# Optimization experiments

Hardware: AMD Instinct MI355X
Metric: run time of the kernel (lower is better)

Reference implementation:

```python
import jax, jax.numpy as jnp
import numpy as np

B, S, H = 1, 2048, 1024
NH, KVH, HD = 16, 4, 64
E, TOPK, F = 8, 2, 2048
EPS = 1e-5
THETA = 10000.0


def setup_inputs() -> dict:
    key = jax.random.key(0)
    ks = jax.random.split(key, 12)
    s = 0.02
    return {
        "hidden_states": jax.random.normal(ks[0], (B, S, H), jnp.float32),
        "position_ids": jnp.arange(S, dtype=jnp.int64).reshape(1, S),
        "ln1_w": jnp.ones((H,), jnp.float32),
        "ln2_w": jnp.ones((H,), jnp.float32),
        "wq": jax.random.normal(ks[1], (NH * HD, H), jnp.float32) * s,
        "wk": jax.random.normal(ks[2], (KVH * HD, H), jnp.float32) * s,
        "wv": jax.random.normal(ks[3], (KVH * HD, H), jnp.float32) * s,
        "wo": jax.random.normal(ks[4], (H, NH * HD), jnp.float32) * s,
        "gate_w": jax.random.normal(ks[5], (E, H), jnp.float32) * s,
        "w1": jax.random.normal(ks[6], (E, F, H), jnp.float32) * s,
        "w2": jax.random.normal(ks[7], (E, H, F), jnp.float32) * s,
        "w3": jax.random.normal(ks[8], (E, F, H), jnp.float32) * s,
    }


def rmsnorm(x, w, eps=EPS):
    xf = x.astype(jnp.float32)
    v = jnp.mean(xf * xf, axis=-1, keepdims=True)
    return (xf * jax.lax.rsqrt(v + eps)).astype(x.dtype) * w


def rotate_half(x):
    x1, x2 = jnp.split(x, 2, axis=-1)
    return jnp.concatenate([-x2, x1], axis=-1)


def attention(x, position_ids, wq, wk, wv, wo):
    q = (x @ wq.T).reshape(B, S, NH, HD).transpose(0, 2, 1, 3)   # [B,NH,S,HD]
    k = (x @ wk.T).reshape(B, S, KVH, HD).transpose(0, 2, 1, 3)  # [B,KVH,S,HD]
    v = (x @ wv.T).reshape(B, S, KVH, HD).transpose(0, 2, 1, 3)
    inv_freq = 1.0 / (THETA ** (jnp.arange(0, HD, 2, dtype=jnp.float32) / HD))
    ang = position_ids.astype(jnp.float32)[:, :, None] * inv_freq  # [B,S,HD/2]
    emb = jnp.concatenate([ang, ang], axis=-1)                     # [B,S,HD]
    cos = jnp.cos(emb)[:, None]                                    # [B,1,S,HD]
    sin = jnp.sin(emb)[:, None]
    q = q * cos + rotate_half(q) * sin
    k = k * cos + rotate_half(k) * sin
    rep = NH // KVH
    k = jnp.repeat(k, rep, axis=1)
    v = jnp.repeat(v, rep, axis=1)
    scores = jnp.einsum("bhqd,bhkd->bhqk", q, k) / np.sqrt(HD).astype(np.float32)
    causal = jnp.tril(jnp.ones((S, S), bool))
    scores = jnp.where(causal, scores, jnp.finfo(scores.dtype).min)
    attn = jax.nn.softmax(scores, axis=-1)
    ctx = jnp.einsum("bhqk,bhkd->bhqd", attn, v)
    ctx = ctx.transpose(0, 2, 1, 3).reshape(B, S, NH * HD)
    return ctx @ wo.T


def moe(x, gate_w, w1, w2, w3):
    xt = x.reshape(-1, H)                                  # [T,H]
    router_logits = xt @ gate_w.T                          # [T,E]
    probs = jax.nn.softmax(router_logits.astype(jnp.float32), axis=-1)
    topw, topi = jax.lax.top_k(probs, TOPK)                # [T,K]
    topw = topw / jnp.sum(topw, axis=-1, keepdims=True)
    topw = topw.astype(x.dtype)
    # combine weights per expert: [T,E]
    cw = jnp.sum(topw[..., None] * jax.nn.one_hot(topi, E, dtype=x.dtype), axis=1)
    h1 = jnp.einsum("th,efh->etf", xt, w1)
    h3 = jnp.einsum("th,efh->etf", xt, w3)
    g = jax.nn.silu(h1) * h3                               # [E,T,F]
    y = jnp.einsum("etf,ehf->eth", g, w2)                  # [E,T,H]
    out = jnp.einsum("eth,te->th", y, cw)
    return out.reshape(B, S, H), router_logits


def reference(hidden_states, position_ids, ln1_w, ln2_w, wq, wk, wv, wo,
              gate_w, w1, w2, w3):
    residual = hidden_states
    h = rmsnorm(hidden_states, ln1_w)
    h = attention(h, position_ids, wq, wk, wv, wo)
    h = residual + h
    residual = h
    h = rmsnorm(h, ln2_w)
    h, router_logits = moe(h, gate_w, w1, w2, w3)
    h = residual + h
    return h, router_logits
```

## Files before the change

### kernel.cpp

```cpp
#include <hip/hip_runtime.h>
#include <hip/hip_bf16.h>
#include <cstdint>

typedef unsigned short u16;
typedef __attribute__((ext_vector_type(8))) short bh8;
typedef __attribute__((ext_vector_type(4))) short sh4;
typedef __attribute__((ext_vector_type(4))) float fx4;

#define NTOK 2048
#define HDIM 1024
#define NE 8
#define FDIM 2048

#define VMCNT(n) asm volatile("s_waitcnt vmcnt(" #n ")" ::: "memory")
#define LGKM0()  asm volatile("s_waitcnt lgkmcnt(0)" ::: "memory")
#define SBAR()   __builtin_amdgcn_s_barrier()
#define SCB()    __builtin_amdgcn_sched_barrier(0)

__device__ __forceinline__ u16 f2bf(float f) {
    __hip_bfloat16 h = __float2bfloat16(f);
    return __builtin_bit_cast(u16, h);
}

__device__ __forceinline__ void gll16(const void* g, void* l) {
    __builtin_amdgcn_global_load_lds(
        (const __attribute__((address_space(1))) void*)g,
        (__attribute__((address_space(3))) void*)l, 16, 0, 0);
}

#define N8_WQ 131072
#define N8_WK 32768
#define N8_WV 32768
#define N8_WO 131072
#define N8_W  2097152
#define B0q 0
#define B1k (B0q + N8_WQ)
#define B2v (B1k + N8_WK)
#define B3o (B2v + N8_WV)
#define B4a (B3o + N8_WO)
#define B5b (B4a + N8_W)
#define B6c (B5b + N8_W)
#define N8TOT (B6c + N8_W)
#define N8QKVO B4a
#define N8_W13 (2 * N8_W)

__device__ __forceinline__ void conv8_nt(const float* __restrict__ src, size_t li,
                                         u16* __restrict__ dst, size_t di) {
    const fx4 a = __builtin_nontemporal_load((const fx4*)&src[li]);
    const fx4 b = __builtin_nontemporal_load((const fx4*)&src[li + 4]);
    bh8 o;
    #pragma unroll
    for (int j = 0; j < 4; ++j) {
        o[j]     = (short)f2bf(a[j]);
        o[j + 4] = (short)f2bf(b[j]);
    }
    __builtin_nontemporal_store(o, (bh8*)&dst[di]);
}

__device__ __forceinline__ void conv8(const float* __restrict__ src, size_t li,
                                      u16* __restrict__ dst, size_t di) {
    const fx4 a = *(const fx4*)&src[li];
    const fx4 b = *(const fx4*)&src[li + 4];
    bh8 o;
    #pragma unroll
    for (int j = 0; j < 4; ++j) {
        o[j]     = (short)f2bf(a[j]);
        o[j + 4] = (short)f2bf(b[j]);
    }
    *(bh8*)&dst[di] = o;
}

__global__ __launch_bounds__(256)
void prologue_k(const float* __restrict__ wq, const float* __restrict__ wk,
                const float* __restrict__ wv, const float* __restrict__ wo,
                u16* __restrict__ arena,
                float* __restrict__ cosT, float* __restrict__ sinT,
                const float* __restrict__ X, const float* __restrict__ W,
                u16* __restrict__ O) {
    const int bid = blockIdx.x;
    const int tid = threadIdx.x;
    if (bid < 256) {
        int i = bid * 256 + tid;
        const int stride = 256 * 256;
        for (; i < N8QKVO; i += stride) {
            const float* src;
            int base;
            if (i < B1k)      { src = wq; base = B0q; }
            else if (i < B2v) { src = wk; base = B1k; }
            else if (i < B3o) { src = wv; base = B2v; }
            else              { src = wo; base = B3o; }
            conv8(src, (size_t)(i - base) * 8, arena, (size_t)i * 8);
        }
        return;
    }
    if (bid < 512) {
        const int idx = (bid - 256) * 256 + tid;
        const int t = idx >> 5, i = idx & 31;
        const float freq = powf(10000.0f, -(float)i * (1.0f / 32.0f));
        const float ang = (float)t * freq;
        float s, c;
        sincosf(ang, &s, &c);
        cosT[idx] = c;
        sinT[idx] = s;
        return;
    }
    const int t = bid - 512;
    const fx4 v = *(const fx4*)&X[(size_t)t * HDIM + tid * 4];
    float ss = v[0]*v[0] + v[1]*v[1] + v[2]*v[2] + v[3]*v[3];
    #pragma unroll
    for (int o = 1; o < 64; o <<= 1) ss += __shfl_xor(ss, o);
    __shared__ float red[4];
    if ((tid & 63) == 0) red[tid >> 6] = ss;
    __syncthreads();
    const float inv = rsqrtf((red[0] + red[1] + red[2] + red[3]) * (1.0f / HDIM) + 1e-5f);
    const fx4 w = *(const fx4*)&W[tid * 4];
    sh4 o4;
    #pragma unroll
    for (int i = 0; i < 4; ++i) o4[i] = (short)f2bf(v[i] * inv * w[i]);
    *(sh4*)&O[(size_t)t * HDIM + tid * 4] = o4;
}

__global__ __launch_bounds__(256)
void rmsnorm2_router_k(const float* __restrict__ X, const float* __restrict__ W,
                       const float* __restrict__ GW, u16* __restrict__ O,
                       float* __restrict__ LOGI) {
    const int t = blockIdx.x;
    const int tid = threadIdx.x;
    const fx4 v = *(const fx4*)&X[(size_t)t * HDIM + tid * 4];
    float ss = v[0]*v[0] + v[1]*v[1] + v[2]*v[2] + v[3]*v[3];
    #pragma unroll
    for (int o = 1; o < 64; o <<= 1) ss += __shfl_xor(ss, o);
    __shared__ float red[4];
    if ((tid & 63) == 0) red[tid >> 6] = ss;
    __syncthreads();
    const float inv = rsqrtf((red[0] + red[1] + red[2] + red[3]) * (1.0f / HDIM) + 1e-5f);
    const fx4 w = *(const fx4*)&W[tid * 4];
    fx4 xn;
    #pragma unroll
    for (int i = 0; i < 4; ++i) xn[i] = v[i] * inv * w[i];
    sh4 o4;
    #pragma unroll
    for (int i = 0; i < 4; ++i) o4[i] = (short)f2bf(xn[i]);
    *(sh4*)&O[(size_t)t * HDIM + tid * 4] = o4;

    float part[NE];
    #pragma unroll
    for (int e = 0; e < NE; ++e) {
        const fx4 g = *(const fx4*)&GW[(size_t)e * HDIM + tid * 4];
        part[e] = g[0]*xn[0] + g[1]*xn[1] + g[2]*xn[2] + g[3]*xn[3];
    }
    #pragma unroll
    for (int e = 0; e < NE; ++e)
        #pragma unroll
        for (int o = 1; o < 64; o <<= 1) part[e] += __shfl_xor(part[e], o);
    __shared__ float red8[4][NE];
    if ((tid & 63) == 0) {
        #pragma unroll
        for (int e = 0; e < NE; ++e) red8[tid >> 6][e] = part[e];
    }
    __syncthreads();
    if (tid < NE)
        LOGI[(size_t)t * NE + tid] = red8[0][tid] + red8[1][tid] + red8[2][tid] + red8[3][tid];
}

__global__ __launch_bounds__(256)
void router_topk_k(const float* __restrict__ LOGI, int* __restrict__ counts,
                   int* __restrict__ tokslot, float* __restrict__ wtb) {
    const int t = blockIdx.x * 256 + threadIdx.x;
    float l[NE];
    #pragma unroll
    for (int e = 0; e < NE; ++e) l[e] = LOGI[(size_t)t * NE + e];
    int i0 = 0;
    #pragma unroll
    for (int e = 1; e < NE; ++e) if (l[e] > l[i0]) i0 = e;
    int i1 = (i0 == 0) ? 1 : 0;
    #pragma unroll
    for (int e = 0; e < NE; ++e) if (e != i0 && l[e] > l[i1]) i1 = e;
    float e1 = __expf(l[i1] - l[i0]);
    float w0 = 1.0f / (1.0f + e1);
    float w1 = 1.0f - w0;
    int p0 = atomicAdd(&counts[i0], 1);
    tokslot[i0 * NTOK + p0] = t * 2;
    wtb[i0 * NTOK + p0] = w0;
    int p1 = atomicAdd(&counts[i1], 1);
    tokslot[i1 * NTOK + p1] = t * 2 + 1;
    wtb[i1 * NTOK + p1] = w1;
}

__global__ __launch_bounds__(256)
void qkv_gemm_k(const u16* __restrict__ A, const u16* __restrict__ Bw,
                u16* __restrict__ Qb, u16* __restrict__ Kb, u16* __restrict__ VTb,
                const float* __restrict__ cosT, const float* __restrict__ sinT) {
    __shared__ u16 As[4][64 * 32];
    __shared__ u16 Bs[4][64 * 32];

    const int tid = threadIdx.x;
    const int lane = tid & 63;
    const int wid = tid >> 6;
    const int lrow = lane & 15, lgrp = lane >> 4;
    const int wm = wid * 16;
    const int soff = (lgrp ^ ((lrow >> 1) & 3)) * 8;

    const int m0 = blockIdx.y * 64;
    const int nt = blockIdx.x;
    const int n0 = nt * 64;

    const int gseg = ((tid & 3) ^ ((tid >> 3) & 3)) * 8;
    const u16* apg = A + (size_t)(m0 + (tid >> 2)) * 1024 + gseg;
    const u16* bpg = Bw + (size_t)(n0 + (tid >> 2)) * 1024 + gseg;

    fx4 acc[4];
    #pragma unroll
    for (int i = 0; i < 4; ++i) acc[i] = fx4{0.f, 0.f, 0.f, 0.f};

#define G_STG(BUF, KK) gll16(apg + (KK), &As[BUF][wid * 512]); \
                       gll16(bpg + (KK), &Bs[BUF][wid * 512]);
#define G_CMP(BUF)                                                             \
    {                                                                          \
        const bh8 af = *(const bh8*)&As[BUF][(wm + lrow) * 32 + soff];         \
        _Pragma("unroll")                                                      \
        for (int ni = 0; ni < 4; ++ni) {                                       \
            const bh8 bf = *(const bh8*)&Bs[BUF][(ni * 16 + lrow) * 32 + soff];\
            acc[ni] = __builtin_amdgcn_mfma_f32_16x16x32_bf16(af, bf, acc[ni], 0, 0, 0); \
        }                                                                      \
    }
#define G_PHASE(BUF_ST, KOFF, BUF_CM)                                          \
    { const int kn = (k0 + (KOFF) < 1024) ? k0 + (KOFF) : 0; G_STG(BUF_ST, kn) } \
    VMCNT(6); SBAR(); SCB();                                                   \
    G_CMP(BUF_CM)                                                              \
    LGKM0(); SBAR();

    G_STG(0, 0) G_STG(1, 32) G_STG(2, 64)
    for (int k0 = 0; k0 < 1024; k0 += 128) {
        G_PHASE(3, 96, 0)
        G_PHASE(0, 128, 1)
        G_PHASE(1, 160, 2)
        G_PHASE(2, 192, 3)
    }
    VMCNT(0);
#undef G_STG
#undef G_CMP
#undef G_PHASE

    if (nt < 20) {
        u16* dst = (nt < 16) ? Qb : Kb;
        const int N = (nt < 16) ? 1024 : 256;
        const int cb = (nt < 16) ? n0 : (nt - 16) * 64;
        #pragma unroll
        for (int j = 0; j < 4; ++j) {
            const int r = m0 + wm + lgrp * 4 + j;
            #pragma unroll
            for (int ni = 0; ni < 2; ++ni) {
                const int d = ni * 16 + lrow;
                const float cv = cosT[r * 32 + d];
                const float sv = sinT[r * 32 + d];
                const float v0 = acc[ni][j];
                const float v1 = acc[ni + 2][j];
                dst[(size_t)r * N + cb + d]      = f2bf(v0 * cv - v1 * sv);
                dst[(size_t)r * N + cb + d + 32] = f2bf(v1 * cv + v0 * sv);
            }
        }
    } else {
        #pragma unroll
        for (int ni = 0; ni < 4; ++ni) {
            const int c = (nt - 20) * 64 + ni * 16 + lrow;
            const int r = m0 + wm + lgrp * 4;
            sh4 o4;
            #pragma unroll
            for (int j = 0; j < 4; ++j) o4[j] = (short)f2bf(acc[ni][j]);
            *(sh4*)&VTb[(size_t)c * NTOK + r] = o4;
        }
    }
}

template<int EPI>
__global__ __launch_bounds__(256)
void gemm_bt(const u16* __restrict__ A, const u16* __restrict__ B,
             u16* __restrict__ Cb, float* __restrict__ Cf,
             const int N, const int K,
             const float* __restrict__ aux0, const float* __restrict__ aux1) {
    __shared__ u16 As[4][64 * 32];
    __shared__ u16 Bs[4][64 * 32];

    const int tid = threadIdx.x;
    const int lane = tid & 63;
    const int wid = tid >> 6;
    const int lrow = lane & 15, lgrp = lane >> 4;
    const int wm = wid * 16;
    const int soff = (lgrp ^ ((lrow >> 1) & 3)) * 8;

    const int m0 = blockIdx.y * 64;
    const int n0 = blockIdx.x * 64;

    const int gseg = ((tid & 3) ^ ((tid >> 3) & 3)) * 8;
    const u16* apg = A + (size_t)(m0 + (tid >> 2)) * K + gseg;
    const u16* bpg = B + (size_t)(n0 + (tid >> 2)) * K + gseg;

    fx4 acc[4];
    #pragma unroll
    for (int i = 0; i < 4; ++i) acc[i] = fx4{0.f, 0.f, 0.f, 0.f};

#define G_STG(BUF, KK) gll16(apg + (KK), &As[BUF][wid * 512]); \
                       gll16(bpg + (KK), &Bs[BUF][wid * 512]);
#define G_CMP(BUF)                                                             \
    {                                                                          \
        const bh8 af = *(const bh8*)&As[BUF][(wm + lrow) * 32 + soff];         \
        _Pragma("unroll")                                                      \
        for (int ni = 0; ni < 4; ++ni) {                                       \
            const bh8 bf = *(const bh8*)&Bs[BUF][(ni * 16 + lrow) * 32 + soff];\
            acc[ni] = __builtin_amdgcn_mfma_f32_16x16x32_bf16(af, bf, acc[ni], 0, 0, 0); \
        }                                                                      \
    }
#define G_PHASE(BUF_ST, KOFF, BUF_CM)                                          \
    { const int kn = (k0 + (KOFF) < K) ? k0 + (KOFF) : 0; G_STG(BUF_ST, kn) }  \
    VMCNT(6); SBAR(); SCB();                                                   \
    G_CMP(BUF_CM)                                                              \
    LGKM0(); SBAR();

    G_STG(0, 0) G_STG(1, 32) G_STG(2, 64)
    for (int k0 = 0; k0 < K; k0 += 128) {
        G_PHASE(3, 96, 0)
        G_PHASE(0, 128, 1)
        G_PHASE(1, 160, 2)
        G_PHASE(2, 192, 3)
    }
    VMCNT(0);
#undef G_STG
#undef G_CMP
#undef G_PHASE

    #pragma unroll
    for (int j = 0; j < 4; ++j) {
        const int r = m0 + wm + lgrp * 4 + j;
        #pragma unroll
        for (int ni = 0; ni < 4; ++ni) {
            const int c = n0 + ni * 16 + lrow;
            const float v = acc[ni][j];
            if (EPI == 1) Cf[(size_t)r * N + c] = v + aux0[(size_t)r * N + c];
        }
    }
}

__global__ __launch_bounds__(256)
void attn_conv_k(const u16* __restrict__ Q, const u16* __restrict__ Kg,
                 const u16* __restrict__ VTg, float* __restrict__ pacc,
                 float* __restrict__ pl,
                 const float* __restrict__ w1, const float* __restrict__ w3,
                 u16* __restrict__ arena_moe) {
    if (blockIdx.z >= 4) {
        const int bid = (blockIdx.z - 4) * 512 + blockIdx.y * 32 + blockIdx.x;
        const int stride = 1024 * 256;
        int i = bid * 256 + threadIdx.x;
        #pragma unroll 1
        for (int k = 0; k < 4; ++k) {
            #pragma unroll
            for (int u = 0; u < 4; ++u) {
                const int ii = i + u * stride;
                const float* s = (ii < N8_W) ? w1 : w3;
                const size_t li = (size_t)(ii < N8_W ? ii : ii - N8_W) * 8;
                const size_t di = (size_t)(ii < N8_W ? ii : ii + N8_W) * 8;
                conv8_nt(s, li, arena_moe, di);
            }
            i += 4 * stride;
        }
        return;
    }

    const int qt = blockIdx.x;
    const int h = blockIdx.y;
    const int c = blockIdx.z;
    if (c * 8 > qt) return;
    const int t0 = c * 8;
    const int tend = min(qt + 1, t0 + 8);
    const int kvh = h >> 2;

    const int tid = threadIdx.x;
    const int lane = tid & 63;
    const int wid = tid >> 6;
    const int lrow = lane & 15, lgrp = lane >> 4;

    __shared__ u16 Ks[64 * 66];
    __shared__ u16 Vs[64 * 66];
    __shared__ u16 Ps[4][16 * 66];

    const int qbase = qt * 64 + wid * 16;

    bh8 qf[2];
    #pragma unroll
    for (int kf = 0; kf < 2; ++kf)
        qf[kf] = *(const bh8*)&Q[(size_t)(qbase + lrow) * 1024 + h * 64 + kf * 32 + lgrp * 8];

    fx4 acc[4];
    #pragma unroll
    for (int ni = 0; ni < 4; ++ni) acc[ni] = fx4{0.f, 0.f, 0.f, 0.f};
    float lsum[4];
    #pragma unroll
    for (int j = 0; j < 4; ++j) lsum[j] = 0.f;

    const int srow = tid >> 2;
    const int sseg = (tid & 3) * 16;

    size_t gk = (size_t)(t0 * 64 + srow) * 256 + kvh * 64 + sseg;
    size_t gv = (size_t)(kvh * 64 + srow) * NTOK + t0 * 64 + sseg;
    bh8 kva = *(const bh8*)&Kg[gk];
    bh8 kvb = *(const bh8*)&Kg[gk + 8];
    bh8 vva = *(const bh8*)&VTg[gv];
    bh8 vvb = *(const bh8*)&VTg[gv + 8];

    for (int it = t0; it < tend; ++it) {
        const int kv0 = it * 64;
        __syncthreads();
        *(bh8*)&Ks[srow * 66 + sseg]     = kva;
        *(bh8*)&Ks[srow * 66 + sseg + 8] = kvb;
        *(bh8*)&Vs[srow * 66 + sseg]     = vva;
        *(bh8*)&Vs[srow * 66 + sseg + 8] = vvb;
        __syncthreads();

        const int itn = (it + 1 < tend) ? it + 1 : it;
        const size_t gk2 = (size_t)(itn * 64 + srow) * 256 + kvh * 64 + sseg;
        const size_t gv2 = (size_t)(kvh * 64 + srow) * NTOK + itn * 64 + sseg;
        kva = *(const bh8*)&Kg[gk2];
        kvb = *(const bh8*)&Kg[gk2 + 8];
        vva = *(const bh8*)&VTg[gv2];
        vvb = *(const bh8*)&VTg[gv2 + 8];

        fx4 s[4];
        #pragma unroll
        for (int nf = 0; nf < 4; ++nf) s[nf] = fx4{0.f, 0.f, 0.f, 0.f};
        #pragma unroll
        for (int kf = 0; kf < 2; ++kf) {
            #pragma unroll
            for (int nf = 0; nf < 4; ++nf) {
                const bh8 kfr = *(const bh8*)&Ks[(nf * 16 + lrow) * 66 + kf * 32 + lgrp * 8];
                s[nf] = __builtin_amdgcn_mfma_f32_16x16x32_bf16(qf[kf], kfr, s[nf], 0, 0, 0);
            }
        }

        #pragma unroll
        for (int nf = 0; nf < 4; ++nf)
            #pragma unroll
            for (int j = 0; j < 4; ++j) {
                const int qr = qbase + lgrp * 4 + j;
                const int kp = kv0 + nf * 16 + lrow;
                float p = __expf(fmaf(s[nf][j], 0.125f, -24.0f));
                p = (kp > qr) ? 0.f : p;
                s[nf][j] = p;
                lsum[j] += p;
            }

        u16* pw = Ps[wid];
        #pragma unroll
        for (int nf = 0; nf < 4; ++nf)
            #pragma unroll
            for (int j = 0; j < 4; ++j)
                pw[(lgrp * 4 + j) * 66 + nf * 16 + lrow] = f2bf(s[nf][j]);

        #pragma unroll
        for (int kf = 0; kf < 2; ++kf) {
            const bh8 pa = *(const bh8*)&pw[lrow * 66 + kf * 32 + lgrp * 8];
            #pragma unroll
            for (int ni = 0; ni < 4; ++ni) {
                const bh8 vb = *(const bh8*)&Vs[(ni * 16 + lrow) * 66 + kf * 32 + lgrp * 8];
                acc[ni] = __builtin_amdgcn_mfma_f32_16x16x32_bf16(pa, vb, acc[ni], 0, 0, 0);
            }
        }
    }

    #pragma unroll
    for (int j = 0; j < 4; ++j) {
        float l = lsum[j];
        #pragma unroll
        for (int o = 1; o < 16; o <<= 1) l += __shfl_xor(l, o);
        lsum[j] = l;
    }

    #pragma unroll
    for (int j = 0; j < 4; ++j) {
        const int r = qbase + lgrp * 4 + j;
        const size_t base = ((size_t)(h * NTOK + r) * 4 + c) * 64;
        #pragma unroll
        for (int ni = 0; ni < 4; ++ni)
            pacc[base + ni * 16 + lrow] = acc[ni][j];
        if (lrow == 0)
            pl[(size_t)(h * NTOK + r) * 4 + c] = lsum[j];
    }
}

__global__ __launch_bounds__(256)
void attn_combine_k(const float* __restrict__ pacc, const float* __restrict__ pl,
                    u16* __restrict__ O) {
    const int idx = blockIdx.x * 4 + (threadIdx.x >> 6);
    const int d = threadIdx.x & 63;
    const int h = idx >> 11;
    const int qrow = idx & 2047;
    const int nch = (qrow >> 9) + 1;

    float den = 0.f, num = 0.f;
    for (int c = 0; c < nch; ++c) {
        den += pl[(size_t)idx * 4 + c];
        num += pacc[((size_t)idx * 4 + c) * 64 + d];
    }
    O[(size_t)qrow * 1024 + h * 64 + d] = f2bf(num / den);
}

__global__ __launch_bounds__(256)
void moe_up_k(const u16* __restrict__ X, const u16* __restrict__ W1b,
              const u16* __restrict__ W3b, const int* __restrict__ counts,
              const int* __restrict__ tokslot, u16* __restrict__ G,
              const float* __restrict__ w2, u16* __restrict__ w2b) {
    if (blockIdx.z == 8) {
        const int bid = blockIdx.y * 16 + blockIdx.x;
        const int stride = 512 * 256;
        int i = bid * 256 + threadIdx.x;
        #pragma unroll 1
        for (int k = 0; k < 4; ++k) {
            #pragma unroll
            for (int u = 0; u < 4; ++u)
                conv8_nt(w2, (size_t)(i + u * stride) * 8, w2b, (size_t)(i + u * stride) * 8);
            i += 4 * stride;
        }
        return;
    }

    const int e = blockIdx.z;
    const int cnt = counts[e];
    const int m0 = blockIdx.y * 64;
    if (m0 >= cnt) return;
    const int n0 = blockIdx.x * 128;

    __shared__ u16 As[4][64 * 32];
    __shared__ u16 B1s[4][128 * 32];
    __shared__ u16 B3s[4][128 * 32];

    const int tid = threadIdx.x;
    const int lane = tid & 63, wid = tid >> 6;
    const int wm = (wid >> 1) * 32, wn = (wid & 1) * 64;
    const int lrow = lane & 15, lgrp = lane >> 4;
    const int soff = (lgrp ^ ((lrow >> 1) & 3)) * 8;

    const int gseg = ((tid & 3) ^ ((tid >> 3) & 3)) * 8;
    const int arow = m0 + (tid >> 2);
    const int tok = (arow < cnt) ? (tokslot[e * NTOK + arow] >> 1) : 0;
    const u16* apg = X + (size_t)tok * HDIM + gseg;
    const size_t eoff = (size_t)e * FDIM * HDIM;
    const u16* b1pg = W1b + eoff + (size_t)(n0 + (tid >> 2)) * HDIM + gseg;
    const u16* b3pg = W3b + eoff + (size_t)(n0 + (tid >> 2)) * HDIM + gseg;
    const size_t rr = (size_t)64 * HDIM;

    fx4 acc1[2][4], acc3[2][4];
    #pragma unroll
    for (int i = 0; i < 2; ++i)
        #pragma unroll
        for (int j = 0; j < 4; ++j) {
            acc1[i][j] = fx4{0.f, 0.f, 0.f, 0.f};
            acc3[i][j] = fx4{0.f, 0.f, 0.f, 0.f};
        }

#define U_STG(BUF, KK)                                          \
    gll16(apg + (KK), &As[BUF][wid * 512]);                     \
    gll16(b1pg + (KK), &B1s[BUF][wid * 512]);                   \
    gll16(b1pg + rr + (KK), &B1s[BUF][2048 + wid * 512]);       \
    gll16(b3pg + (KK), &B3s[BUF][wid * 512]);                   \
    gll16(b3pg + rr + (KK), &B3s[BUF][2048 + wid * 512]);

#define U_CMP(BUF)                                                                   \
    {                                                                                \
        bh8 af[2], b1f[4], b3f[4];                                                   \
        _Pragma("unroll")                                                            \
        for (int mi = 0; mi < 2; ++mi)                                               \
            af[mi] = *(const bh8*)&As[BUF][(wm + mi * 16 + lrow) * 32 + soff];       \
        _Pragma("unroll")                                                            \
        for (int ni = 0; ni < 4; ++ni) {                                             \
            b1f[ni] = *(const bh8*)&B1s[BUF][(wn + ni * 16 + lrow) * 32 + soff];     \
            b3f[ni] = *(const bh8*)&B3s[BUF][(wn + ni * 16 + lrow) * 32 + soff];     \
        }                                                                            \
        _Pragma("unroll")                                                            \
        for (int mi = 0; mi < 2; ++mi)                                               \
            _Pragma("unroll")                                                        \
            for (int ni = 0; ni < 4; ++ni) {                                         \
                acc1[mi][ni] = __builtin_amdgcn_mfma_f32_16x16x32_bf16(af[mi], b1f[ni], acc1[mi][ni], 0, 0, 0); \
                acc3[mi][ni] = __builtin_amdgcn_mfma_f32_16x16x32_bf16(af[mi], b3f[ni], acc3[mi][ni], 0, 0, 0); \
            }                                                                        \
    }

#define U_PHASE(BUF_ST, KOFF, BUF_CM)                                          \
    { const int kn = (k0 + (KOFF) < HDIM) ? k0 + (KOFF) : 0; U_STG(BUF_ST, kn) } \
    VMCNT(15); SBAR(); SCB();                                                  \
    U_CMP(BUF_CM)                                                              \
    LGKM0(); SBAR();

    U_STG(0, 0) U_STG(1, 32) U_STG(2, 64)
    for (int k0 = 0; k0 < HDIM; k0 += 128) {
        U_PHASE(3, 96, 0)
        U_PHASE(0, 128, 1)
        U_PHASE(1, 160, 2)
        U_PHASE(2, 192, 3)
    }
    VMCNT(0);
#undef U_STG
#undef U_CMP
#undef U_PHASE

    #pragma unroll
    for (int mi = 0; mi < 2; ++mi)
        #pragma unroll
        for (int j = 0; j < 4; ++j) {
            const int r = m0 + wm + mi * 16 + lgrp * 4 + j;
            if (r < cnt) {
                #pragma unroll
                for (int ni = 0; ni < 4; ++ni) {
                    const int c = n0 + wn + ni * 16 + lrow;
                    const float h1 = acc1[mi][ni][j];
                    const float h3 = acc3[mi][ni][j];
                    const float gv = h1 / (1.0f + __expf(-h1)) * h3;
                    G[((size_t)e * NTOK + r) * FDIM + c] = f2bf(gv);
                }
            }
        }
}

__global__ __launch_bounds__(256)
void moe_down_k(const u16* __restrict__ G, const u16* __restrict__ W2b,
                const int* __restrict__ counts, const int* __restrict__ tokslot,
                const float* __restrict__ wtb, float* __restrict__ MO) {
    const int e = blockIdx.z;
    const int cnt = counts[e];
    const int m0 = blockIdx.y * 64;
    if (m0 >= cnt) return;
    const int n0 = blockIdx.x * 64;

    __shared__ u16 As[4][64 * 32];
    __shared__ u16 Bs[4][64 * 32];

    const int tid = threadIdx.x;
    const int lane = tid & 63;
    const int wid = tid >> 6;
    const int lrow = lane & 15, lgrp = lane >> 4;
    const int wm = wid * 16;
    const int soff = (lgrp ^ ((lrow >> 1) & 3)) * 8;

    const int gseg = ((tid & 3) ^ ((tid >> 3) & 3)) * 8;
    const u16* apg = G + ((size_t)e * NTOK + m0 + (tid >> 2)) * FDIM + gseg;
    const u16* bpg = W2b + (size_t)e * HDIM * FDIM + (size_t)(n0 + (tid >> 2)) * FDIM + gseg;

    fx4 acc[4];
    #pragma unroll
    for (int i = 0; i < 4; ++i) acc[i] = fx4{0.f, 0.f, 0.f, 0.f};

#define D_STG(BUF, KK) gll16(apg + (KK), &As[BUF][wid * 512]); \
                       gll16(bpg + (KK), &Bs[BUF][wid * 512]);
#define D_CMP(BUF)                                                             \
    {                                                                          \
        const bh8 af = *(const bh8*)&As[BUF][(wm + lrow) * 32 + soff];         \
        _Pragma("unroll")                                                      \
        for (int ni = 0; ni < 4; ++ni) {                                       \
            const bh8 bf = *(const bh8*)&Bs[BUF][(ni * 16 + lrow) * 32 + soff];\
            acc[ni] = __builtin_amdgcn_mfma_f32_16x16x32_bf16(af, bf, acc[ni], 0, 0, 0); \
        }                                                                      \
    }
#define D_PHASE(BUF_ST, KOFF, BUF_CM)                                          \
    { const int kn = (k0 + (KOFF) < FDIM) ? k0 + (KOFF) : 0; D_STG(BUF_ST, kn) } \
    VMCNT(6); SBAR(); SCB();                                                   \
    D_CMP(BUF_CM)                                                              \
    LGKM0(); SBAR();

    D_STG(0, 0) D_STG(1, 32) D_STG(2, 64)
    for (int k0 = 0; k0 < FDIM; k0 += 128) {
        D_PHASE(3, 96, 0)
        D_PHASE(0, 128, 1)
        D_PHASE(1, 160, 2)
        D_PHASE(2, 192, 3)
    }
    VMCNT(0);
#undef D_STG
#undef D_CMP
#undef D_PHASE

    #pragma unroll
    for (int j = 0; j < 4; ++j) {
        const int r = m0 + wm + lgrp * 4 + j;
        if (r < cnt) {
            const int ts = tokslot[e * NTOK + r];
            const float wgt = wtb[e * NTOK + r];
            const int tt = ts >> 1;
            const int sl = ts & 1;
            #pragma unroll
            for (int ni = 0; ni < 4; ++ni) {
                const int c = n0 + ni * 16 + lrow;
                MO[((size_t)sl * NTOK + tt) * HDIM + c] = acc[ni][j] * wgt;
            }
        }
    }
}

__global__ __launch_bounds__(256)
void final_add_k(const float* __restrict__ A, const float* __restrict__ B0,
                 const float* __restrict__ B1, float* __restrict__ O) {
    const size_t i = ((size_t)blockIdx.x * 256 + threadIdx.x) * 4;
    const fx4 a = *(const fx4*)&A[i];
    const fx4 b = *(const fx4*)&B0[i];
    const fx4 c = *(const fx4*)&B1[i];
    fx4 r;
    #pragma unroll
    for (int k = 0; k < 4; ++k) r[k] = a[k] + b[k] + c[k];
    *(fx4*)&O[i] = r;
}

extern "C" void kernel_launch(void* const* d_in, const int* in_sizes, int n_in,
                              void* d_out, int out_size, void* d_ws, size_t ws_size,
                              hipStream_t stream) {
    const float* x   = (const float*)d_in[0];
    const float* ln1 = (const float*)d_in[2];
    const float* ln2 = (const float*)d_in[3];
    const float* wq  = (const float*)d_in[4];
    const float* wk  = (const float*)d_in[5];
    const float* wv  = (const float*)d_in[6];
    const float* wo  = (const float*)d_in[7];
    const float* gw  = (const float*)d_in[8];
    const float* w1  = (const float*)d_in[9];
    const float* w2  = (const float*)d_in[10];
    const float* w3  = (const float*)d_in[11];

    float* out_h = (float*)d_out;
    float* out_logits = out_h + (size_t)NTOK * HDIM;

    uint8_t* wsb = (uint8_t*)d_ws;
    size_t off = 0;
    auto alloc = [&](size_t bytes) -> void* {
        void* ptr = wsb + off;
        off = (off + bytes + 255) & ~(size_t)255;
        return ptr;
    };
    u16*   xn1    = (u16*)alloc((size_t)NTOK * HDIM * 2);
    u16*   qb     = (u16*)alloc((size_t)NTOK * 1024 * 2);
    u16*   kb     = (u16*)alloc((size_t)NTOK * 256 * 2);
    u16*   vbt    = (u16*)alloc((size_t)256 * NTOK * 2);
    u16*   ctxb   = (u16*)alloc((size_t)NTOK * 1024 * 2);
    float* hattn  = (float*)alloc((size_t)NTOK * HDIM * 4);
    u16*   xn2    = (u16*)alloc((size_t)NTOK * HDIM * 2);
    float* cosT   = (float*)alloc((size_t)NTOK * 32 * 4);
    float* sinT   = (float*)alloc((size_t)NTOK * 32 * 4);
    int*   counts = (int*)alloc(NE * 4);
    int*   tokslot= (int*)alloc((size_t)NE * NTOK * 4);
    float* wtb    = (float*)alloc((size_t)NE * NTOK * 4);
    u16*   gbuf   = (u16*)alloc((size_t)NE * NTOK * FDIM * 2);
    float* moeb   = (float*)alloc((size_t)2 * NTOK * HDIM * 4);
    u16*   arena  = (u16*)alloc((size_t)N8TOT * 8 * 2);
    u16*   w1b    = arena + (size_t)B4a * 8;
    u16*   w2b    = arena + (size_t)B5b * 8;
    u16*   w3b    = arena + (size_t)B6c * 8;
    u16*   wob    = arena + (size_t)B3o * 8;

    float* pacc = (float*)gbuf;
    float* pl   = pacc + (size_t)16 * NTOK * 4 * 64;

    hipMemsetAsync(counts, 0, NE * 4, stream);

    prologue_k<<<2560, 256, 0, stream>>>(wq, wk, wv, wo, arena, cosT, sinT, x, ln1, xn1);
    qkv_gemm_k<<<dim3(24, 32), 256, 0, stream>>>(xn1, arena, qb, kb, vbt, cosT, sinT);
    attn_conv_k<<<dim3(32, 16, 6), 256, 0, stream>>>(qb, kb, vbt, pacc, pl,
                                                     w1, w3, arena + (size_t)B4a * 8);
    attn_combine_k<<<8192, 256, 0, stream>>>(pacc, pl, ctxb);
    gemm_bt<1><<<dim3(16, 32), 256, 0, stream>>>(ctxb, wob, nullptr, hattn, 1024, 1024, x, nullptr);
    rmsnorm2_router_k<<<NTOK, 256, 0, stream>>>(hattn, ln2, gw, xn2, out_logits);
    router_topk_k<<<8, 256, 0, stream>>>(out_logits, counts, tokslot, wtb);
    moe_up_k<<<dim3(16, 32, NE + 1), 256, 0, stream>>>(xn2, w1b, w3b, counts, tokslot, gbuf,
                                                       w2, w2b);
    moe_down_k<<<dim3(16, 32, NE), 256, 0, stream>>>(gbuf, w2b, counts, tokslot, wtb, moeb);
    final_add_k<<<NTOK, 256, 0, stream>>>(hattn, moeb, moeb + (size_t)NTOK * HDIM, out_h);
}
```

Before: 338.7 us.

## Use atomic work-stealing for weight conversion inside attention and MoE-up kernels

New measurement: 414.5 us. 22.4% more time.

```diff
diff --git a/kernel.cpp b/kernel.cpp
--- a/kernel.cpp
+++ b/kernel.cpp
@@ -43,6 +43,9 @@
 #define N8TOT (B6c + N8_W)
 #define N8QKVO B4a
 #define N8_W13 (2 * N8_W)
+#define CHUNK_G8 1024
+#define NCHUNK_W13 (N8_W13 / CHUNK_G8)
+#define NCHUNK_W2  (N8_W / CHUNK_G8)
 
 __device__ __forceinline__ void conv8_nt(const float* __restrict__ src, size_t li,
                                          u16* __restrict__ dst, size_t di) {
@@ -346,143 +349,143 @@
                  const u16* __restrict__ VTg, float* __restrict__ pacc,
                  float* __restrict__ pl,
                  const float* __restrict__ w1, const float* __restrict__ w3,
-                 u16* __restrict__ arena_moe) {
-    if (blockIdx.z >= 4) {
-        const int bid = (blockIdx.z - 4) * 512 + blockIdx.y * 32 + blockIdx.x;
-        const int stride = 1024 * 256;
-        int i = bid * 256 + threadIdx.x;
-        #pragma unroll 1
-        for (int k = 0; k < 4; ++k) {
-            #pragma unroll
-            for (int u = 0; u < 4; ++u) {
-                const int ii = i + u * stride;
-                const float* s = (ii < N8_W) ? w1 : w3;
-                const size_t li = (size_t)(ii < N8_W ? ii : ii - N8_W) * 8;
-                const size_t di = (size_t)(ii < N8_W ? ii : ii + N8_W) * 8;
-                conv8_nt(s, li, arena_moe, di);
-            }
-            i += 4 * stride;
-        }
-        return;
-    }
-
+                 u16* __restrict__ arena_moe, int* __restrict__ ctr) {
     const int qt = blockIdx.x;
     const int h = blockIdx.y;
     const int c = blockIdx.z;
-    if (c * 8 > qt) return;
-    const int t0 = c * 8;
-    const int tend = min(qt + 1, t0 + 8);
-    const int kvh = h >> 2;
-
     const int tid = threadIdx.x;
-    const int lane = tid & 63;
-    const int wid = tid >> 6;
-    const int lrow = lane & 15, lgrp = lane >> 4;
-
-    __shared__ u16 Ks[64 * 66];
-    __shared__ u16 Vs[64 * 66];
-    __shared__ u16 Ps[4][16 * 66];
-
-    const int qbase = qt * 64 + wid * 16;
-
-    bh8 qf[2];
-    #pragma unroll
-    for (int kf = 0; kf < 2; ++kf)
-        qf[kf] = *(const bh8*)&Q[(size_t)(qbase + lrow) * 1024 + h * 64 + kf * 32 + lgrp * 8];
-
-    fx4 acc[4];
-    #pragma unroll
-    for (int ni = 0; ni < 4; ++ni) acc[ni] = fx4{0.f, 0.f, 0.f, 0.f};
-    float lsum[4];
-    #pragma unroll
-    for (int j = 0; j < 4; ++j) lsum[j] = 0.f;
-
-    const int srow = tid >> 2;
-    const int sseg = (tid & 3) * 16;
-
-    size_t gk = (size_t)(t0 * 64 + srow) * 256 + kvh * 64 + sseg;
-    size_t gv = (size_t)(kvh * 64 + srow) * NTOK + t0 * 64 + sseg;
-    bh8 kva = *(const bh8*)&Kg[gk];
-    bh8 kvb = *(const bh8*)&Kg[gk + 8];
-    bh8 vva = *(const bh8*)&VTg[gv];
-    bh8 vvb = *(const bh8*)&VTg[gv + 8];
-
-    for (int it = t0; it < tend; ++it) {
-        const int kv0 = it * 64;
+    __shared__ int sh_ch;
+
+    if (c * 8 <= qt) {
+        const int t0 = c * 8;
+        const int tend = min(qt + 1, t0 + 8);
+        const int kvh = h >> 2;
+
+        const int lane = tid & 63;
+        const int wid = tid >> 6;
+        const int lrow = lane & 15, lgrp = lane >> 4;
+
+        __shared__ u16 Ks[64 * 66];
+        __shared__ u16 Vs[64 * 66];
+        __shared__ u16 Ps[4][16 * 66];
+
+        const int qbase = qt * 64 + wid * 16;
+
+        bh8 qf[2];
+        #pragma unroll
+        for (int kf = 0; kf < 2; ++kf)
+            qf[kf] = *(const bh8*)&Q[(size_t)(qbase + lrow) * 1024 + h * 64 + kf * 32 + lgrp * 8];
+
+        fx4 acc[4];
+        #pragma unroll
+        for (int ni = 0; ni < 4; ++ni) acc[ni] = fx4{0.f, 0.f, 0.f, 0.f};
+        float lsum[4];
+        #pragma unroll
+        for (int j = 0; j < 4; ++j) lsum[j] = 0.f;
+
+        const int srow = tid >> 2;
+        const int sseg = (tid & 3) * 16;
+
+        size_t gk = (size_t)(t0 * 64 + srow) * 256 + kvh * 64 + sseg;
+        size_t gv = (size_t)(kvh * 64 + srow) * NTOK + t0 * 64 + sseg;
+        bh8 kva = *(const bh8*)&Kg[gk];
+        bh8 kvb = *(const bh8*)&Kg[gk + 8];
+        bh8 vva = *(const bh8*)&VTg[gv];
+        bh8 vvb = *(const bh8*)&VTg[gv + 8];
+
+        for (int it = t0; it < tend; ++it) {
+            const int kv0 = it * 64;
+            __syncthreads();
+            *(bh8*)&Ks[srow * 66 + sseg]     = kva;
+            *(bh8*)&Ks[srow * 66 + sseg + 8] = kvb;
+            *(bh8*)&Vs[srow * 66 + sseg]     = vva;
+            *(bh8*)&Vs[srow * 66 + sseg + 8] = vvb;
+            __syncthreads();
+
+            const int itn = (it + 1 < tend) ? it + 1 : it;
+            const size_t gk2 = (size_t)(itn * 64 + srow) * 256 + kvh * 64 + sseg;
+            const size_t gv2 = (size_t)(kvh * 64 + srow) * NTOK + itn * 64 + sseg;
+            kva = *(const bh8*)&Kg[gk2];
+            kvb = *(const bh8*)&Kg[gk2 + 8];
+            vva = *(const bh8*)&VTg[gv2];
+            vvb = *(const bh8*)&VTg[gv2 + 8];
+
+            fx4 s[4];
+            #pragma unroll
+            for (int nf = 0; nf < 4; ++nf) s[nf] = fx4{0.f, 0.f, 0.f, 0.f};
+            #pragma unroll
+            for (int kf = 0; kf < 2; ++kf) {
+                #pragma unroll
+                for (int nf = 0; nf < 4; ++nf) {
+                    const bh8 kfr = *(const bh8*)&Ks[(nf * 16 + lrow) * 66 + kf * 32 + lgrp * 8];
+                    s[nf] = __builtin_amdgcn_mfma_f32_16x16x32_bf16(qf[kf], kfr, s[nf], 0, 0, 0);
+                }
+            }
+
+            #pragma unroll
+            for (int nf = 0; nf < 4; ++nf)
+                #pragma unroll
+                for (int j = 0; j < 4; ++j) {
+                    const int qr = qbase + lgrp * 4 + j;
+                    const int kp = kv0 + nf * 16 + lrow;
+                    float p = __expf(fmaf(s[nf][j], 0.125f, -24.0f));
+                    p = (kp > qr) ? 0.f : p;
+                    s[nf][j] = p;
+                    lsum[j] += p;
+                }
+
+            u16* pw = Ps[wid];
+            #pragma unroll
+            for (int nf = 0; nf < 4; ++nf)
+                #pragma unroll
+                for (int j = 0; j < 4; ++j)
+                    pw[(lgrp * 4 + j) * 66 + nf * 16 + lrow] = f2bf(s[nf][j]);
+
+            #pragma unroll
+            for (int kf = 0; kf < 2; ++kf) {
+                const bh8 pa = *(const bh8*)&pw[lrow * 66 + kf * 32 + lgrp * 8];
+                #pragma unroll
+                for (int ni = 0; ni < 4; ++ni) {
+                    const bh8 vb = *(const bh8*)&Vs[(ni * 16 + lrow) * 66 + kf * 32 + lgrp * 8];
+                    acc[ni] = __builtin_amdgcn_mfma_f32_16x16x32_bf16(pa, vb, acc[ni], 0, 0, 0);
+                }
+            }
+        }
+
+        #pragma unroll
+        for (int j = 0; j < 4; ++j) {
+            float l = lsum[j];
+            #pragma unroll
+            for (int o = 1; o < 16; o <<= 1) l += __shfl_xor(l, o);
+            lsum[j] = l;
+        }
+
+        #pragma unroll
+        for (int j = 0; j < 4; ++j) {
+            const int r = qbase + lgrp * 4 + j;
+            const size_t base = ((size_t)(h * NTOK + r) * 4 + c) * 64;
+            #pragma unroll
+            for (int ni = 0; ni < 4; ++ni)
+                pacc[base + ni * 16 + lrow] = acc[ni][j];
+            if (lrow == 0)
+                pl[(size_t)(h * NTOK + r) * 4 + c] = lsum[j];
+        }
+    }
+
+    for (;;) {
+        if (tid == 0) sh_ch = atomicAdd(ctr, 1);
         __syncthreads();
-        *(bh8*)&Ks[srow * 66 + sseg]     = kva;
-        *(bh8*)&Ks[srow * 66 + sseg + 8] = kvb;
-        *(bh8*)&Vs[srow * 66 + sseg]     = vva;
-        *(bh8*)&Vs[srow * 66 + sseg + 8] = vvb;
+        const int ch = sh_ch;
         __syncthreads();
-
-        const int itn = (it + 1 < tend) ? it + 1 : it;
-        const size_t gk2 = (size_t)(itn * 64 + srow) * 256 + kvh * 64 + sseg;
-        const size_t gv2 = (size_t)(kvh * 64 + srow) * NTOK + itn * 64 + sseg;
-        kva = *(const bh8*)&Kg[gk2];
-        kvb = *(const bh8*)&Kg[gk2 + 8];
-        vva = *(const bh8*)&VTg[gv2];
-        vvb = *(const bh8*)&VTg[gv2 + 8];
-
-        fx4 s[4];
-        #pragma unroll
-        for (int nf = 0; nf < 4; ++nf) s[nf] = fx4{0.f, 0.f, 0.f, 0.f};
-        #pragma unroll
-        for (int kf = 0; kf < 2; ++kf) {
-            #pragma unroll
-            for (int nf = 0; nf < 4; ++nf) {
-                const bh8 kfr = *(const bh8*)&Ks[(nf * 16 + lrow) * 66 + kf * 32 + lgrp * 8];
-                s[nf] = __builtin_amdgcn_mfma_f32_16x16x32_bf16(qf[kf], kfr, s[nf], 0, 0, 0);
-            }
-        }
-
-        #pragma unroll
-        for (int nf = 0; nf < 4; ++nf)
-            #pragma unroll
-            for (int j = 0; j < 4; ++j) {
-                const int qr = qbase + lgrp * 4 + j;
-                const int kp = kv0 + nf * 16 + lrow;
-                float p = __expf(fmaf(s[nf][j], 0.125f, -24.0f));
-                p = (kp > qr) ? 0.f : p;
-                s[nf][j] = p;
-                lsum[j] += p;
-            }
-
-        u16* pw = Ps[wid];
-        #pragma unroll
-        for (int nf = 0; nf < 4; ++nf)
-            #pragma unroll
-            for (int j = 0; j < 4; ++j)
-                pw[(lgrp * 4 + j) * 66 + nf * 16 + lrow] = f2bf(s[nf][j]);
-
-        #pragma unroll
-        for (int kf = 0; kf < 2; ++kf) {
-            const bh8 pa = *(const bh8*)&pw[lrow * 66 + kf * 32 + lgrp * 8];
-            #pragma unroll
-            for (int ni = 0; ni < 4; ++ni) {
-                const bh8 vb = *(const bh8*)&Vs[(ni * 16 + lrow) * 66 + kf * 32 + lgrp * 8];
-                acc[ni] = __builtin_amdgcn_mfma_f32_16x16x32_bf16(pa, vb, acc[ni], 0, 0, 0);
-            }
-        }
-    }
-
-    #pragma unroll
-    for (int j = 0; j < 4; ++j) {
-        float l = lsum[j];
-        #pragma unroll
-        for (int o = 1; o < 16; o <<= 1) l += __shfl_xor(l, o);
-        lsum[j] = l;
-    }
-
-    #pragma unroll
-    for (int j = 0; j < 4; ++j) {
-        const int r = qbase + lgrp * 4 + j;
-        const size_t base = ((size_t)(h * NTOK + r) * 4 + c) * 64;
-        #pragma unroll
-        for (int ni = 0; ni < 4; ++ni)
-            pacc[base + ni * 16 + lrow] = acc[ni][j];
-        if (lrow == 0)
-            pl[(size_t)(h * NTOK + r) * 4 + c] = lsum[j];
+        if (ch >= NCHUNK_W13) break;
+        #pragma unroll
+        for (int u = 0; u < 4; ++u) {
+            const int ii = ch * CHUNK_G8 + u * 256 + tid;
+            const float* s = (ii < N8_W) ? w1 : w3;
+            const size_t li = (size_t)(ii < N8_W ? ii : ii - N8_W) * 8;
+            const size_t di = (size_t)(ii < N8_W ? ii : ii + N8_W) * 8;
+            conv8_nt(s, li, arena_moe, di);
+        }
     }
 }
 
@@ -507,54 +510,43 @@
 void moe_up_k(const u16* __restrict__ X, const u16* __restrict__ W1b,
               const u16* __restrict__ W3b, const int* __restrict__ counts,
               const int* __restrict__ tokslot, u16* __restrict__ G,
-              const float* __restrict__ w2, u16* __restrict__ w2b) {
-    if (blockIdx.z == 8) {
-        const int bid = blockIdx.y * 16 + blockIdx.x;
-        const int stride = 512 * 256;
-        int i = bid * 256 + threadIdx.x;
-        #pragma unroll 1
-        for (int k = 0; k < 4; ++k) {
-            #pragma unroll
-            for (int u = 0; u < 4; ++u)
-                conv8_nt(w2, (size_t)(i + u * stride) * 8, w2b, (size_t)(i + u * stride) * 8);
-            i += 4 * stride;
-        }
-        return;
-    }
+              const float* __restrict__ w2, u16* __restrict__ w2b,
+              int* __restrict__ ctr) {
+    const int tid = threadIdx.x;
+    __shared__ int sh_ch;
 
     const int e = blockIdx.z;
     const int cnt = counts[e];
     const int m0 = blockIdx.y * 64;
-    if (m0 >= cnt) return;
-    const int n0 = blockIdx.x * 128;
-
-    __shared__ u16 As[4][64 * 32];
-    __shared__ u16 B1s[4][128 * 32];
-    __shared__ u16 B3s[4][128 * 32];
-
-    const int tid = threadIdx.x;
-    const int lane = tid & 63, wid = tid >> 6;
-    const int wm = (wid >> 1) * 32, wn = (wid & 1) * 64;
-    const int lrow = lane & 15, lgrp = lane >> 4;
-    const int soff = (lgrp ^ ((lrow >> 1) & 3)) * 8;
-
-    const int gseg = ((tid & 3) ^ ((tid >> 3) & 3)) * 8;
-    const int arow = m0 + (tid >> 2);
-    const int tok = (arow < cnt) ? (tokslot[e * NTOK + arow] >> 1) : 0;
-    const u16* apg = X + (size_t)tok * HDIM + gseg;
-    const size_t eoff = (size_t)e * FDIM * HDIM;
-    const u16* b1pg = W1b + eoff + (size_t)(n0 + (tid >> 2)) * HDIM + gseg;
-    const u16* b3pg = W3b + eoff + (size_t)(n0 + (tid >> 2)) * HDIM + gseg;
-    const size_t rr = (size_t)64 * HDIM;
-
-    fx4 acc1[2][4], acc3[2][4];
-    #pragma unroll
-    for (int i = 0; i < 2; ++i)
-        #pragma unroll
-        for (int j = 0; j < 4; ++j) {
-            acc1[i][j] = fx4{0.f, 0.f, 0.f, 0.f};
-            acc3[i][j] = fx4{0.f, 0.f, 0.f, 0.f};
-        }
+    if (m0 < cnt) {
+        const int n0 = blockIdx.x * 128;
+
+        __shared__ u16 As[4][64 * 32];
+        __shared__ u16 B1s[4][128 * 32];
+        __shared__ u16 B3s[4][128 * 32];
+
+        const int lane = tid & 63, wid = tid >> 6;
+        const int wm = (wid >> 1) * 32, wn = (wid & 1) * 64;
+        const int lrow = lane & 15, lgrp = lane >> 4;
+        const int soff = (lgrp ^ ((lrow >> 1) & 3)) * 8;
+
+        const int gseg = ((tid & 3) ^ ((tid >> 3) & 3)) * 8;
+        const int arow = m0 + (tid >> 2);
+        const int tok = (arow < cnt) ? (tokslot[e * NTOK + arow] >> 1) : 0;
+        const u16* apg = X + (size_t)tok * HDIM + gseg;
+        const size_t eoff = (size_t)e * FDIM * HDIM;
+        const u16* b1pg = W1b + eoff + (size_t)(n0 + (tid >> 2)) * HDIM + gseg;
+        const u16* b3pg = W3b + eoff + (size_t)(n0 + (tid >> 2)) * HDIM + gseg;
+        const size_t rr = (size_t)64 * HDIM;
+
+        fx4 acc1[2][4], acc3[2][4];
+        #pragma unroll
+        for (int i = 0; i < 2; ++i)
+            #pragma unroll
+            for (int j = 0; j < 4; ++j) {
+                acc1[i][j] = fx4{0.f, 0.f, 0.f, 0.f};
+                acc3[i][j] = fx4{0.f, 0.f, 0.f, 0.f};
+            }
 
 #define U_STG(BUF, KK)                                          \
     gll16(apg + (KK), &As[BUF][wid * 512]);                     \
@@ -589,34 +581,48 @@
     U_CMP(BUF_CM)                                                              \
     LGKM0(); SBAR();
 
-    U_STG(0, 0) U_STG(1, 32) U_STG(2, 64)
-    for (int k0 = 0; k0 < HDIM; k0 += 128) {
-        U_PHASE(3, 96, 0)
-        U_PHASE(0, 128, 1)
-        U_PHASE(1, 160, 2)
-        U_PHASE(2, 192, 3)
-    }
-    VMCNT(0);
+        U_STG(0, 0) U_STG(1, 32) U_STG(2, 64)
+        for (int k0 = 0; k0 < HDIM; k0 += 128) {
+            U_PHASE(3, 96, 0)
+            U_PHASE(0, 128, 1)
+            U_PHASE(1, 160, 2)
+            U_PHASE(2, 192, 3)
+        }
+        VMCNT(0);
 #undef U_STG
 #undef U_CMP
 #undef U_PHASE
 
-    #pragma unroll
-    for (int mi = 0; mi < 2; ++mi)
-        #pragma unroll
-        for (int j = 0; j < 4; ++j) {
-            const int r = m0 + wm + mi * 16 + lgrp * 4 + j;
-            if (r < cnt) {
-                #pragma unroll
-                for (int ni = 0; ni < 4; ++ni) {
-                    const int c = n0 + wn + ni * 16 + lrow;
-                    const float h1 = acc1[mi][ni][j];
-                    const float h3 = acc3[mi][ni][j];
-                    const float gv = h1 / (1.0f + __expf(-h1)) * h3;
-                    G[((size_t)e * NTOK + r) * FDIM + c] = f2bf(gv);
+        #pragma unroll
+        for (int mi = 0; mi < 2; ++mi)
+            #pragma unroll
+            for (int j = 0; j < 4; ++j) {
+                const int r = m0 + wm + mi * 16 + lgrp * 4 + j;
+                if (r < cnt) {
+                    #pragma unroll
+                    for (int ni = 0; ni < 4; ++ni) {
+                        const int c = n0 + wn + ni * 16 + lrow;
+                        const float h1 = acc1[mi][ni][j];
+                        const float h3 = acc3[mi][ni][j];
+                        const float gv = h1 / (1.0f + __expf(-h1)) * h3;
+                        G[((size_t)e * NTOK + r) * FDIM + c] = f2bf(gv);
+                    }
                 }
             }
-        }
+    }
+
+    for (;;) {
+        if (tid == 0) sh_ch = atomicAdd(ctr, 1);
+        __syncthreads();
+        const int ch = sh_ch;
+        __syncthreads();
+        if (ch >= NCHUNK_W2) break;
+        #pragma unroll
+        for (int u = 0; u < 4; ++u) {
+            const int ii = ch * CHUNK_G8 + u * 256 + tid;
+            conv8_nt(w2, (size_t)ii * 8, w2b, (size_t)ii * 8);
+        }
+    }
 }
 
 __global__ __launch_bounds__(256)
@@ -741,6 +747,7 @@
     float* cosT   = (float*)alloc((size_t)NTOK * 32 * 4);
     float* sinT   = (float*)alloc((size_t)NTOK * 32 * 4);
     int*   counts = (int*)alloc(NE * 4);
+    int*   ctrs   = (int*)alloc(2 * 4);
     int*   tokslot= (int*)alloc((size_t)NE * NTOK * 4);
     float* wtb    = (float*)alloc((size_t)NE * NTOK * 4);
     u16*   gbuf   = (u16*)alloc((size_t)NE * NTOK * FDIM * 2);
@@ -755,17 +762,19 @@
     float* pl   = pacc + (size_t)16 * NTOK * 4 * 64;
 
     hipMemsetAsync(counts, 0, NE * 4, stream);
+    hipMemsetAsync(ctrs, 0, 2 * 4, stream);
 
     prologue_k<<<2560, 256, 0, stream>>>(wq, wk, wv, wo, arena, cosT, sinT, x, ln1, xn1);
     qkv_gemm_k<<<dim3(24, 32), 256, 0, stream>>>(xn1, arena, qb, kb, vbt, cosT, sinT);
-    attn_conv_k<<<dim3(32, 16, 6), 256, 0, stream>>>(qb, kb, vbt, pacc, pl,
-                                                     w1, w3, arena + (size_t)B4a * 8);
+    attn_conv_k<<<dim3(32, 16, 4), 256, 0, stream>>>(qb, kb, vbt, pacc, pl,
+                                                     w1, w3, arena + (size_t)B4a * 8,
+                                                     ctrs);
     attn_combine_k<<<8192, 256, 0, stream>>>(pacc, pl, ctxb);
     gemm_bt<1><<<dim3(16, 32), 256, 0, stream>>>(ctxb, wob, nullptr, hattn, 1024, 1024, x, nullptr);
     rmsnorm2_router_k<<<NTOK, 256, 0, stream>>>(hattn, ln2, gw, xn2, out_logits);
     router_topk_k<<<8, 256, 0, stream>>>(out_logits, counts, tokslot, wtb);
-    moe_up_k<<<dim3(16, 32, NE + 1), 256, 0, stream>>>(xn2, w1b, w3b, counts, tokslot, gbuf,
-                                                       w2, w2b);
+    moe_up_k<<<dim3(16, 32, NE), 256, 0, stream>>>(xn2, w1b, w3b, counts, tokslot, gbuf,
+                                                   w2, w2b, ctrs + 1);
     moe_down_k<<<dim3(16, 32, NE), 256, 0, stream>>>(gbuf, w2b, counts, tokslot, wtb, moeb);
     final_add_k<<<NTOK, 256, 0, stream>>>(hattn, moeb, moeb + (size_t)NTOK * HDIM, out_h);
 }
```

## Fuse top-k routing into rmsnorm and scatter MoE output via atomics

Applied to the files above, without the earlier changes.

After: 368.2 us. 8.7% more time.

```diff
diff --git a/kernel.cpp b/kernel.cpp
--- a/kernel.cpp
+++ b/kernel.cpp
@@ -123,10 +123,13 @@
 __global__ __launch_bounds__(256)
 void rmsnorm2_router_k(const float* __restrict__ X, const float* __restrict__ W,
                        const float* __restrict__ GW, u16* __restrict__ O,
-                       float* __restrict__ LOGI) {
+                       float* __restrict__ LOGI, float* __restrict__ OUT,
+                       int* __restrict__ counts, int* __restrict__ tokslot,
+                       float* __restrict__ wtb) {
     const int t = blockIdx.x;
     const int tid = threadIdx.x;
     const fx4 v = *(const fx4*)&X[(size_t)t * HDIM + tid * 4];
+    *(fx4*)&OUT[(size_t)t * HDIM + tid * 4] = v;
     float ss = v[0]*v[0] + v[1]*v[1] + v[2]*v[2] + v[3]*v[3];
     #pragma unroll
     for (int o = 1; o < 64; o <<= 1) ss += __shfl_xor(ss, o);
@@ -161,30 +164,27 @@
     __syncthreads();
     if (tid < NE)
         LOGI[(size_t)t * NE + tid] = red8[0][tid] + red8[1][tid] + red8[2][tid] + red8[3][tid];
-}
-
-__global__ __launch_bounds__(256)
-void router_topk_k(const float* __restrict__ LOGI, int* __restrict__ counts,
-                   int* __restrict__ tokslot, float* __restrict__ wtb) {
-    const int t = blockIdx.x * 256 + threadIdx.x;
-    float l[NE];
-    #pragma unroll
-    for (int e = 0; e < NE; ++e) l[e] = LOGI[(size_t)t * NE + e];
-    int i0 = 0;
-    #pragma unroll
-    for (int e = 1; e < NE; ++e) if (l[e] > l[i0]) i0 = e;
-    int i1 = (i0 == 0) ? 1 : 0;
-    #pragma unroll
-    for (int e = 0; e < NE; ++e) if (e != i0 && l[e] > l[i1]) i1 = e;
-    float e1 = __expf(l[i1] - l[i0]);
-    float w0 = 1.0f / (1.0f + e1);
-    float w1 = 1.0f - w0;
-    int p0 = atomicAdd(&counts[i0], 1);
-    tokslot[i0 * NTOK + p0] = t * 2;
-    wtb[i0 * NTOK + p0] = w0;
-    int p1 = atomicAdd(&counts[i1], 1);
-    tokslot[i1 * NTOK + p1] = t * 2 + 1;
-    wtb[i1 * NTOK + p1] = w1;
+    if (tid == 0) {
+        float l[NE];
+        #pragma unroll
+        for (int e = 0; e < NE; ++e)
+            l[e] = red8[0][e] + red8[1][e] + red8[2][e] + red8[3][e];
+        int i0 = 0;
+        #pragma unroll
+        for (int e = 1; e < NE; ++e) if (l[e] > l[i0]) i0 = e;
+        int i1 = (i0 == 0) ? 1 : 0;
+        #pragma unroll
+        for (int e = 0; e < NE; ++e) if (e != i0 && l[e] > l[i1]) i1 = e;
+        const float e1 = __expf(l[i1] - l[i0]);
+        const float w0 = 1.0f / (1.0f + e1);
+        const float w1 = 1.0f - w0;
+        const int p0 = atomicAdd(&counts[i0], 1);
+        tokslot[i0 * NTOK + p0] = t;
+        wtb[i0 * NTOK + p0] = w0;
+        const int p1 = atomicAdd(&counts[i1], 1);
+        tokslot[i1 * NTOK + p1] = t;
+        wtb[i1 * NTOK + p1] = w1;
+    }
 }
 
 __global__ __launch_bounds__(256)
@@ -540,7 +540,7 @@
 
     const int gseg = ((tid & 3) ^ ((tid >> 3) & 3)) * 8;
     const int arow = m0 + (tid >> 2);
-    const int tok = (arow < cnt) ? (tokslot[e * NTOK + arow] >> 1) : 0;
+    const int tok = (arow < cnt) ? tokslot[e * NTOK + arow] : 0;
     const u16* apg = X + (size_t)tok * HDIM + gseg;
     const size_t eoff = (size_t)e * FDIM * HDIM;
     const u16* b1pg = W1b + eoff + (size_t)(n0 + (tid >> 2)) * HDIM + gseg;
@@ -622,7 +622,7 @@
 __global__ __launch_bounds__(256)
 void moe_down_k(const u16* __restrict__ G, const u16* __restrict__ W2b,
                 const int* __restrict__ counts, const int* __restrict__ tokslot,
-                const float* __restrict__ wtb, float* __restrict__ MO) {
+                const float* __restrict__ wtb, float* __restrict__ OUT) {
     const int e = blockIdx.z;
     const int cnt = counts[e];
     const int m0 = blockIdx.y * 64;
@@ -680,30 +680,15 @@
     for (int j = 0; j < 4; ++j) {
         const int r = m0 + wm + lgrp * 4 + j;
         if (r < cnt) {
-            const int ts = tokslot[e * NTOK + r];
+            const int tt = tokslot[e * NTOK + r];
             const float wgt = wtb[e * NTOK + r];
-            const int tt = ts >> 1;
-            const int sl = ts & 1;
             #pragma unroll
             for (int ni = 0; ni < 4; ++ni) {
                 const int c = n0 + ni * 16 + lrow;
-                MO[((size_t)sl * NTOK + tt) * HDIM + c] = acc[ni][j] * wgt;
+                atomicAdd(&OUT[(size_t)tt * HDIM + c], acc[ni][j] * wgt);
             }
         }
     }
-}
-
-__global__ __launch_bounds__(256)
-void final_add_k(const float* __restrict__ A, const float* __restrict__ B0,
-                 const float* __restrict__ B1, float* __restrict__ O) {
-    const size_t i = ((size_t)blockIdx.x * 256 + threadIdx.x) * 4;
-    const fx4 a = *(const fx4*)&A[i];
-    const fx4 b = *(const fx4*)&B0[i];
-    const fx4 c = *(const fx4*)&B1[i];
-    fx4 r;
-    #pragma unroll
-    for (int k = 0; k < 4; ++k) r[k] = a[k] + b[k] + c[k];
-    *(fx4*)&O[i] = r;
 }
 
 extern "C" void kernel_launch(void* const* d_in, const int* in_sizes, int n_in,
@@ -744,7 +729,6 @@
     int*   tokslot= (int*)alloc((size_t)NE * NTOK * 4);
     float* wtb    = (float*)alloc((size_t)NE * NTOK * 4);
     u16*   gbuf   = (u16*)alloc((size_t)NE * NTOK * FDIM * 2);
-    float* moeb   = (float*)alloc((size_t)2 * NTOK * HDIM * 4);
     u16*   arena  = (u16*)alloc((size_t)N8TOT * 8 * 2);
     u16*   w1b    = arena + (size_t)B4a * 8;
     u16*   w2b    = arena + (size_t)B5b * 8;
@@ -762,10 +746,9 @@
                                                      w1, w3, arena + (size_t)B4a * 8);
     attn_combine_k<<<8192, 256, 0, stream>>>(pacc, pl, ctxb);
     gemm_bt<1><<<dim3(16, 32), 256, 0, stream>>>(ctxb, wob, nullptr, hattn, 1024, 1024, x, nullptr);
-    rmsnorm2_router_k<<<NTOK, 256, 0, stream>>>(hattn, ln2, gw, xn2, out_logits);
-    router_topk_k<<<8, 256, 0, stream>>>(out_logits, counts, tokslot, wtb);
+    rmsnorm2_router_k<<<NTOK, 256, 0, stream>>>(hattn, ln2, gw, xn2, out_logits,
+                                                out_h, counts, tokslot, wtb);
     moe_up_k<<<dim3(16, 32, NE + 1), 256, 0, stream>>>(xn2, w1b, w3b, counts, tokslot, gbuf,
                                                        w2, w2b);
-    moe_down_k<<<dim3(16, 32, NE), 256, 0, stream>>>(gbuf, w2b, counts, tokslot, wtb, moeb);
-    final_add_k<<<NTOK, 256, 0, stream>>>(hattn, moeb, moeb + (size_t)NTOK * HDIM, out_h);
-}
+    moe_down_k<<<dim3(16, 32, NE), 256, 0, stream>>>(gbuf, w2b, counts, tokslot, wtb, out_h);
+}
```
